# Kernel tuning notes

Hardware: AMD Instinct MI355X
Metric: run time of the kernel (lower is better)

## Reference

```python
import jax, jax.numpy as jnp
import numpy as np

N_NODES = 100000
N_EDGES = 1600000
NUM_GRAPHS = 4096
HID = 128
F_IN = 11
F_OUT = 19


def setup_inputs() -> dict:
    key = jax.random.key(0)
    ks = jax.random.split(key, 8)
    x = jax.random.normal(ks[0], (N_NODES, F_IN), dtype=jnp.float32)
    edge_src = jax.random.randint(ks[1], (N_EDGES,), 0, N_NODES)
    edge_dst = jax.random.randint(ks[2], (N_EDGES,), 0, N_NODES)
    batch = jnp.sort(jax.random.randint(ks[3], (N_NODES,), 0, NUM_GRAPHS))
    W1 = jax.random.normal(ks[4], (F_IN, HID), dtype=jnp.float32) / np.sqrt(F_IN)
    b1 = jnp.zeros((HID,), dtype=jnp.float32)
    W2 = jax.random.normal(ks[5], (HID, HID), dtype=jnp.float32) / np.sqrt(HID)
    b2 = jnp.zeros((HID,), dtype=jnp.float32)
    Wlin = jax.random.normal(ks[6], (HID, F_OUT), dtype=jnp.float32) / np.sqrt(HID)
    blin = jnp.zeros((F_OUT,), dtype=jnp.float32)
    return {"x": x, "edge_src": edge_src, "edge_dst": edge_dst, "batch": batch,
            "W1": W1, "b1": b1, "W2": W2, "b2": b2, "Wlin": Wlin, "blin": blin}


def _gcn_conv(x, W, b, src, dst, norm, n_nodes):
    # x: [N, Fin] -> h: [N, Fout]; gather-normalize-scatter over edges (self-loops included in src/dst/norm)
    h = x @ W
    msgs = h[src] * norm[:, None]              # [E+N, Fout]
    out = jax.ops.segment_sum(msgs, dst, num_segments=n_nodes)
    return out + b


def reference(x, edge_src, edge_dst, batch, W1, b1, W2, b2, Wlin, blin):
    n = x.shape[0]
    # add self-loops (GCNConv default)
    loops = jnp.arange(n)
    src = jnp.concatenate([edge_src, loops])
    dst = jnp.concatenate([edge_dst, loops])
    # symmetric normalization deg^-1/2[src] * deg^-1/2[dst], deg computed on dst with self-loops
    deg = jax.ops.segment_sum(jnp.ones_like(dst, dtype=x.dtype), dst, num_segments=n)
    dinv = jnp.where(deg > 0, jax.lax.rsqrt(deg), 0.0)
    norm = dinv[src] * dinv[dst]
    h = _gcn_conv(x, W1, b1, src, dst, norm, n)
    h = jax.nn.relu(h)
    h = _gcn_conv(h, W2, b2, src, dst, norm, n)
    # global mean pool over batch assignment
    sums = jax.ops.segment_sum(h, batch, num_segments=NUM_GRAPHS)
    cnts = jax.ops.segment_sum(jnp.ones((n,), dtype=h.dtype), batch, num_segments=NUM_GRAPHS)
    pooled = sums / jnp.maximum(cnts, 1.0)[:, None]   # [NUM_GRAPHS, HID]
    return pooled @ Wlin + blin                       # [NUM_GRAPHS, F_OUT]
```

## Files before the change

kernel.cpp:

```cpp
#include <hip/hip_runtime.h>
#include <hip/hip_fp16.h>

#define N_NODES 100000
#define N_EDGES 1600000
#define NUM_G   4096
#define HID     128
#define F_IN    11
#define F_PAD   16
#define F_OUT   19

#define NB      256
#define KPB     391
#define BCAP    8192
#define GCAP    1024
#define P01_EPB 2048
#define NBLK_E  782
#define NGBB    16
#define NREG    8
#define REGW    12500
#define GPB     4
#define NAGG    782
#define CH_G    8

__device__ inline void acc_row_f16(float* acc, uint4 u, float w) {
    const __half2* hp = (const __half2*)&u;
#pragma unroll
    for (int i = 0; i < 4; ++i) {
        acc[2 * i]     += __half2float(__low2half(hp[i]))  * w;
        acc[2 * i + 1] += __half2float(__high2half(hp[i])) * w;
    }
}
__device__ inline void add_row_f16(float* acc, uint4 u) {
    const __half2* hp = (const __half2*)&u;
#pragma unroll
    for (int i = 0; i < 4; ++i) {
        acc[2 * i]     += __half2float(__low2half(hp[i]));
        acc[2 * i + 1] += __half2float(__high2half(hp[i]));
    }
}

__global__ void p1_place(const int* __restrict__ src, const int* __restrict__ dst,
                         const int* __restrict__ batch,
                         int* __restrict__ bcur, unsigned int* __restrict__ ebuf,
                         int* __restrict__ gb) {
    if (blockIdx.x >= NBLK_E) {
        int g = (blockIdx.x - NBLK_E) * 256 + threadIdx.x;
        if (g < NUM_G) {
            int lo = 0, hi = N_NODES;
            while (lo < hi) { int m = (lo + hi) >> 1; if (batch[m] < g) lo = m + 1; else hi = m; }
            gb[g] = lo;
            if (g == NUM_G - 1) gb[NUM_G] = N_NODES;
        }
        return;
    }
    __shared__ int h[NB];
    __shared__ int lbase[NB];
    __shared__ int gbase[NB];
    __shared__ int wsum4[4];
    __shared__ int total_s;
    __shared__ unsigned int stage[P01_EPB];
    __shared__ unsigned char sbuck[P01_EPB];
    int tid = threadIdx.x;
    h[tid] = 0;
    __syncthreads();
    unsigned int pk[8]; int bn[8];
    int b0 = blockIdx.x * P01_EPB;
    int e8 = b0 + tid * 8;
    if (e8 + 8 <= N_EDGES) {
        int4 s0 = *(const int4*)(src + e8);
        int4 s1 = *(const int4*)(src + e8 + 4);
        int4 d0 = *(const int4*)(dst + e8);
        int4 d1 = *(const int4*)(dst + e8 + 4);
        int ss[8] = { s0.x, s0.y, s0.z, s0.w, s1.x, s1.y, s1.z, s1.w };
        int dd[8] = { d0.x, d0.y, d0.z, d0.w, d1.x, d1.y, d1.z, d1.w };
#pragma unroll
        for (int k = 0; k < 8; ++k) {
            bn[k] = dd[k] / KPB;
            pk[k] = ((unsigned)ss[k] << 9) | (unsigned)(dd[k] - bn[k] * KPB);
        }
    } else {
#pragma unroll
        for (int k = 0; k < 8; ++k) {
            int e = e8 + k;
            if (e < N_EDGES) {
                int d = dst[e];
                bn[k] = d / KPB;
                pk[k] = ((unsigned)src[e] << 9) | (unsigned)(d - bn[k] * KPB);
            } else bn[k] = -1;
        }
    }
#pragma unroll
    for (int k = 0; k < 8; ++k)
        if (bn[k] >= 0) atomicAdd(&h[bn[k]], 1);
    __syncthreads();
    int c = h[tid];
    gbase[tid] = c ? atomicAdd(&bcur[tid], c) : 0;
    int lane = tid & 63, wv = tid >> 6;
    int sv = c;
#pragma unroll
    for (int off = 1; off < 64; off <<= 1) {
        int n = __shfl_up(sv, off, 64);
        if (lane >= off) sv += n;
    }
    if (lane == 63) wsum4[wv] = sv;
    __syncthreads();
    int woff = 0;
    for (int w = 0; w < wv; ++w) woff += wsum4[w];
    int excl = sv - c + woff;
    lbase[tid] = excl;
    if (tid == NB - 1) total_s = excl + c;
    __syncthreads();
    h[tid] = 0;
    __syncthreads();
#pragma unroll
    for (int k = 0; k < 8; ++k) {
        if (bn[k] >= 0) {
            int r = atomicAdd(&h[bn[k]], 1);
            int p_ = lbase[bn[k]] + r;
            stage[p_] = pk[k];
            sbuck[p_] = (unsigned char)bn[k];
        }
    }
    __syncthreads();
    int total = total_s;
    for (int i = tid; i < total; i += NB) {
        int b = sbuck[i];
        ebuf[(size_t)b * BCAP + gbase[b] + (i - lbase[b])] = stage[i];
    }
}

__global__ void p2_build(const unsigned int* __restrict__ ebuf, const int* __restrict__ bcur,
                         const float* __restrict__ x,
                         int* __restrict__ row_ptr, int* __restrict__ deg,
                         uint2* __restrict__ cw,
                         float* __restrict__ dinv, __half* __restrict__ xp) {
    __shared__ int hist[512];
    __shared__ float ldinv[512];
    __shared__ int wsum[8];
    __shared__ int woff[8];
    int b  = blockIdx.x;
    int t  = threadIdx.x;
    int dbase = b * KPB;
    int nd = N_NODES - dbase; if (nd > KPB) nd = KPB;
    if (t < 512) hist[t] = 0;
    __syncthreads();
    int e0 = b * BCAP;
    int e1 = e0 + bcur[b];
    for (int e = e0 + t; e < e1; e += 1024)
        atomicAdd(&hist[ebuf[e] & 511u], 1);
    __syncthreads();
    int v = 0, sv = 0;
    int lane = t & 63, wv = t >> 6;
    if (t < 512) {
        v = hist[t];
        sv = v;
#pragma unroll
        for (int off = 1; off < 64; off <<= 1) {
            int n = __shfl_up(sv, off, 64);
            if (lane >= off) sv += n;
        }
        if (lane == 63) wsum[wv] = sv;
    }
    __syncthreads();
    if (t == 0) {
        int run = 0;
#pragma unroll
        for (int w = 0; w < 8; ++w) { woff[w] = run; run += wsum[w]; }
    }
    __syncthreads();
    int excl = 0;
    if (t < 512) {
        excl = sv - v + woff[wv];
        float di = rsqrtf(1.0f + (float)v);
        ldinv[t] = di;
        if (t < nd) {
            row_ptr[dbase + t] = e0 + excl;
            deg[dbase + t]     = v;
            dinv[dbase + t]    = di;
        }
    }
    __syncthreads();
    if (t < 512) hist[t] = e0 + excl;
    __syncthreads();
    for (int e = e0 + t; e < e1; e += 1024) {
        unsigned int w = ebuf[e];
        int dl = (int)(w & 511u);
        int pos = atomicAdd(&hist[dl], 1);
        cw[pos] = make_uint2(w >> 9, __float_as_uint(ldinv[dl]));
    }
    for (int idx = t; idx < nd * F_PAD; idx += 1024) {
        int vl = idx >> 4, f = idx & 15;
        int gv = dbase + vl;
        xp[(size_t)gv * F_PAD + f] =
            __float2half_rn((f < F_IN) ? ldinv[vl] * x[(size_t)gv * F_IN + f] : 0.f);
    }
}

__global__ void agg_es8(const __half* __restrict__ xp, const int* __restrict__ row_ptr,
                        const int* __restrict__ deg, const uint2* __restrict__ cw,
                        const float* __restrict__ dinv,
                        const float* __restrict__ W1, const float* __restrict__ b1,
                        __half* __restrict__ Bh,
                        const int* __restrict__ gb,
                        uint2* __restrict__ ewp, int* __restrict__ gro) {
    __shared__ float xs[128][F_PAD];
    __shared__ float W1s[F_IN * HID];
    __shared__ float b1s[HID];
    __shared__ float ds[128];
    __shared__ int cnt[NREG];
    __shared__ int cur[NREG];
    int tid = threadIdx.x;

    if (blockIdx.x < NAGG) {
        for (int i = tid; i < F_IN * HID; i += 256) W1s[i] = W1[i];
        if (tid < HID) b1s[tid] = b1[tid];
        const uint4* xp4 = (const uint4*)xp;
        int v0   = blockIdx.x * 128;
        int v    = v0 + (tid >> 1);
        int lane = tid & 1;
        if (v < N_NODES) {
            if (lane == 0) ds[tid >> 1] = dinv[v];
            float a[8];
#pragma unroll
            for (int k = 0; k < 8; ++k) a[k] = 0.f;
            add_row_f16(a, xp4[(size_t)v * 2 + lane]);
            int j = row_ptr[v], end = j + deg[v];
            for (; j + 3 < end; j += 4) {
                int s0 = cw[j].x, s1 = cw[j + 1].x, s2 = cw[j + 2].x, s3 = cw[j + 3].x;
                uint4 u0 = xp4[(size_t)s0 * 2 + lane];
                uint4 u1 = xp4[(size_t)s1 * 2 + lane];
                uint4 u2 = xp4[(size_t)s2 * 2 + lane];
                uint4 u3 = xp4[(size_t)s3 * 2 + lane];
                add_row_f16(a, u0); add_row_f16(a, u1);
                add_row_f16(a, u2); add_row_f16(a, u3);
            }
            for (; j < end; ++j)
                add_row_f16(a, xp4[(size_t)cw[j].x * 2 + lane]);
#pragma unroll
            for (int k = 0; k < 8; ++k) xs[tid >> 1][lane * 8 + k] = a[k];
        }
        __syncthreads();
        int jf   = tid & 127;
        int half = tid >> 7;
        int nmax = N_NODES - v0; if (nmax > 128) nmax = 128;
        for (int n = half; n < nmax; n += 2) {
            float a = 0.f;
#pragma unroll
            for (int k = 0; k < F_IN; ++k) a += xs[n][k] * W1s[k * HID + jf];
            float dv = ds[n];
            float h = fmaxf(dv * a + b1s[jf], 0.f);
            Bh[(size_t)(v0 + n) * HID + jf] = __float2half_rn(dv * h);
        }
    } else {
        int g = blockIdx.x - NAGG;
        if (tid < NREG) cnt[tid] = 0;
        __syncthreads();
        int r0 = gb[g], r1 = gb[g + 1];
        int bb0 = 0, bb1 = -1;
        if (r1 > r0) { bb0 = r0 / KPB; bb1 = (r1 - 1) / KPB; }
        for (int bb = bb0; bb <= bb1; ++bb) {
            int vlo = r0 > bb * KPB ? r0 : bb * KPB;
            int vhi = r1 < bb * KPB + KPB ? r1 : bb * KPB + KPB;
            int ee0 = row_ptr[vlo];
            int ee1 = row_ptr[vhi - 1] + deg[vhi - 1];
            for (int e = ee0 + tid; e < ee1; e += 256)
                atomicAdd(&cnt[cw[e].x / REGW], 1);
        }
        for (int v = r0 + tid; v < r1; v += 256)
            atomicAdd(&cnt[(unsigned)v / REGW], 1);
        __syncthreads();
        if (tid == 0) {
            int run = g * GCAP;
#pragma unroll
            for (int p = 0; p < NREG; ++p) {
                gro[g * 9 + p] = run;
                cur[p] = run;
                run += cnt[p];
            }
            gro[g * 9 + 8] = run;
        }
        __syncthreads();
        for (int bb = bb0; bb <= bb1; ++bb) {
            int vlo = r0 > bb * KPB ? r0 : bb * KPB;
            int vhi = r1 < bb * KPB + KPB ? r1 : bb * KPB + KPB;
            int ee0 = row_ptr[vlo];
            int ee1 = row_ptr[vhi - 1] + deg[vhi - 1];
            for (int e = ee0 + tid; e < ee1; e += 256) {
                uint2 q = cw[e];
                int pos = atomicAdd(&cur[q.x / REGW], 1);
                ewp[pos] = q;
            }
        }
        for (int v = r0 + tid; v < r1; v += 256) {
            int pos = atomicAdd(&cur[(unsigned)v / REGW], 1);
            ewp[pos] = make_uint2((unsigned)v, __float_as_uint(dinv[v]));
        }
    }
}

__global__ void pool_gather(const __half* __restrict__ Bh,
                            const int* __restrict__ gro,
                            const uint2* __restrict__ ewp,
                            float* __restrict__ part) {
    __shared__ float red[32][HID + 4];
    int b    = blockIdx.x;
    int gset = b >> 3;
    int p    = b & 7;
    int tid  = threadIdx.x;
    int grp  = tid >> 3;
    int lane = tid & 7;
    int g    = gset * GPB + (grp >> 3);
    int q    = grp & 7;
    const uint4* B4 = (const uint4*)Bh;
    float acc[16];
#pragma unroll
    for (int k = 0; k < 16; ++k) acc[k] = 0.f;

    int e0 = gro[g * 9 + p], e1 = gro[g * 9 + p + 1];
    int e = e0 + q;
    for (; e + 8 < e1; e += 16) {
        uint2 q0 = ewp[e], q1 = ewp[e + 8];
        uint4 u00 = B4[(size_t)q0.x * 16 + lane];
        uint4 u01 = B4[(size_t)q0.x * 16 + 8 + lane];
        uint4 u10 = B4[(size_t)q1.x * 16 + lane];
        uint4 u11 = B4[(size_t)q1.x * 16 + 8 + lane];
        float w0 = __uint_as_float(q0.y), w1 = __uint_as_float(q1.y);
        acc_row_f16(acc,     u00, w0);
        acc_row_f16(acc + 8, u01, w0);
        acc_row_f16(acc,     u10, w1);
        acc_row_f16(acc + 8, u11, w1);
    }
    for (; e < e1; e += 8) {
        uint2 q0 = ewp[e];
        uint4 u00 = B4[(size_t)q0.x * 16 + lane];
        uint4 u01 = B4[(size_t)q0.x * 16 + 8 + lane];
        float w0 = __uint_as_float(q0.y);
        acc_row_f16(acc,     u00, w0);
        acc_row_f16(acc + 8, u01, w0);
    }
#pragma unroll
    for (int k = 0; k < 8; ++k) red[grp][lane * 8 + k]      = acc[k];
#pragma unroll
    for (int k = 0; k < 8; ++k) red[grp][64 + lane * 8 + k] = acc[8 + k];
    __syncthreads();
    for (int i = tid; i < GPB * HID; i += 256) {
        int gg = i >> 7, f = i & 127;
        int rb = gg * 8;
        float s = 0.f;
#pragma unroll
        for (int r = 0; r < 8; ++r) s += red[rb + r][f];
        part[(size_t)((gset * GPB + gg) * NREG + p) * HID + f] = s;
    }
}

__global__ void combine_head(const float* __restrict__ part, const int* __restrict__ gb,
                             const float* __restrict__ W2, const float* __restrict__ b2,
                             const float* __restrict__ Wlin, const float* __restrict__ blin,
                             float* __restrict__ out) {
    __shared__ float r[CH_G][HID];
    __shared__ float tt[CH_G][HID + 4];
    __shared__ float bsc[CH_G];
    int g0  = blockIdx.x * CH_G;
    int tid = threadIdx.x;
    int f   = tid & 127;
    int gh  = tid >> 7;
    int q0  = gh * 4;
#pragma unroll
    for (int c = 0; c < 4; ++c) {
        int gg = q0 + c;
        int g  = g0 + gg;
        float s = 0.f;
#pragma unroll
        for (int p = 0; p < NREG; ++p) s += part[(size_t)(g * NREG + p) * HID + f];
        int cnt = gb[g + 1] - gb[g];
        float inv = (cnt > 0) ? 1.0f / (float)cnt : 0.f;
        r[gg][f] = s * inv;
        if (f == 0) bsc[gg] = (cnt > 0) ? 1.0f : 0.f;
    }
    __syncthreads();
    float bf = b2[f];
    float t0 = bf * bsc[q0];
    float t1 = bf * bsc[q0 + 1];
    float t2 = bf * bsc[q0 + 2];
    float t3 = bf * bsc[q0 + 3];
#pragma unroll 4
    for (int k = 0; k < HID; ++k) {
        float w = W2[k * HID + f];
        t0 += r[q0][k] * w;
        t1 += r[q0 + 1][k] * w;
        t2 += r[q0 + 2][k] * w;
        t3 += r[q0 + 3][k] * w;
    }
    tt[q0][f]     = t0;
    tt[q0 + 1][f] = t1;
    tt[q0 + 2][f] = t2;
    tt[q0 + 3][f] = t3;
    __syncthreads();
    if (tid < CH_G * F_OUT) {
        int gg = tid / F_OUT;
        int fo = tid - gg * F_OUT;
        float o = blin[fo];
#pragma unroll 8
        for (int k = 0; k < HID; ++k) o += tt[gg][k] * Wlin[k * F_OUT + fo];
        out[(size_t)(g0 + gg) * F_OUT + fo] = o;
    }
}

extern "C" void kernel_launch(void* const* d_in, const int* in_sizes, int n_in,
                              void* d_out, int out_size, void* d_ws, size_t ws_size,
                              hipStream_t stream) {
    const float* x    = (const float*)d_in[0];
    const int*   esrc = (const int*)  d_in[1];
    const int*   edst = (const int*)  d_in[2];
    const int*   batch= (const int*)  d_in[3];
    const float* W1   = (const float*)d_in[4];
    const float* b1   = (const float*)d_in[5];
    const float* W2   = (const float*)d_in[6];
    const float* b2   = (const float*)d_in[7];
    const float* Wlin = (const float*)d_in[8];
    const float* blin = (const float*)d_in[9];
    float* out = (float*)d_out;

    char* p = (char*)d_ws;
    float*        dinv    = (float*)p;        p += sizeof(float) * N_NODES;
    __half*       xp      = (__half*)p;       p += sizeof(__half) * (size_t)N_NODES * F_PAD;
    __half*       Bh      = (__half*)p;       p += sizeof(__half) * (size_t)N_NODES * HID;
    unsigned int* ebuf    = (unsigned int*)p; p += sizeof(unsigned int) * (size_t)NB * BCAP;
    uint2*        cw      = (uint2*)p;        p += sizeof(uint2) * (size_t)NB * BCAP;
    int*          deg     = (int*)p;          p += sizeof(int) * N_NODES;
    uint2*        ewp     = (uint2*)p;        p += sizeof(uint2) * (size_t)NUM_G * GCAP;
    float*        part    = (float*)p;        p += sizeof(float) * (size_t)NUM_G * NREG * HID;
    int*          row_ptr = (int*)p;          p += sizeof(int) * (N_NODES + 4);
    int*          gb      = (int*)p;          p += sizeof(int) * (NUM_G + 4);
    int*          gro     = (int*)p;          p += sizeof(int) * (NUM_G * 9 + 4);
    int*          bcur    = (int*)p;          p += sizeof(int) * NB;

    hipMemsetAsync(bcur, 0, sizeof(int) * NB, stream);
    p1_place<<<NBLK_E + NGBB, 256, 0, stream>>>(esrc, edst, batch, bcur, ebuf, gb);
    p2_build<<<NB, 1024, 0, stream>>>(ebuf, bcur, x, row_ptr, deg, cw, dinv, xp);

    agg_es8<<<NAGG + NUM_G, 256, 0, stream>>>(xp, row_ptr, deg, cw, dinv, W1, b1, Bh,
                                              gb, ewp, gro);

    pool_gather<<<(NUM_G / GPB) * NREG, 256, 0, stream>>>(Bh, gro, ewp, part);

    combine_head<<<NUM_G / CH_G, 256, 0, stream>>>(part, gb, W2, b2, Wlin, blin, out);
}
```

Before: 207.4 us.

## Stage CSR and graph-edge bucketing in LDS for coalesced global writes

```diff
diff --git a/kernel.cpp b/kernel.cpp
--- a/kernel.cpp
+++ b/kernel.cpp
@@ -138,6 +138,7 @@
     __shared__ float ldinv[512];
     __shared__ int wsum[8];
     __shared__ int woff[8];
+    __shared__ uint2 scw[BCAP];
     int b  = blockIdx.x;
     int t  = threadIdx.x;
     int dbase = b * KPB;
@@ -180,14 +181,18 @@
         }
     }
     __syncthreads();
-    if (t < 512) hist[t] = e0 + excl;
+    if (t < 512) hist[t] = excl;
     __syncthreads();
     for (int e = e0 + t; e < e1; e += 1024) {
         unsigned int w = ebuf[e];
         int dl = (int)(w & 511u);
         int pos = atomicAdd(&hist[dl], 1);
-        cw[pos] = make_uint2(w >> 9, __float_as_uint(ldinv[dl]));
-    }
+        scw[pos] = make_uint2(w >> 9, __float_as_uint(ldinv[dl]));
+    }
+    __syncthreads();
+    int cnt_ = e1 - e0;
+    for (int i = t; i < cnt_; i += 1024)
+        cw[e0 + i] = scw[i];
     for (int idx = t; idx < nd * F_PAD; idx += 1024) {
         int vl = idx >> 4, f = idx & 15;
         int gv = dbase + vl;
@@ -203,23 +208,33 @@
                         __half* __restrict__ Bh,
                         const int* __restrict__ gb,
                         uint2* __restrict__ ewp, int* __restrict__ gro) {
-    __shared__ float xs[128][F_PAD];
-    __shared__ float W1s[F_IN * HID];
-    __shared__ float b1s[HID];
-    __shared__ float ds[128];
+    __shared__ union SBuf {
+        struct {
+            float xs[128][F_PAD];
+            float W1s[F_IN * HID];
+            float b1s[HID];
+            float ds[128];
+        } a;
+        struct {
+            uint2 dat[GCAP];
+            uint2 ord[GCAP];
+            unsigned char reg[GCAP];
+        } s;
+    } sh;
     __shared__ int cnt[NREG];
     __shared__ int cur[NREG];
+    __shared__ int stot;
     int tid = threadIdx.x;
 
     if (blockIdx.x < NAGG) {
-        for (int i = tid; i < F_IN * HID; i += 256) W1s[i] = W1[i];
-        if (tid < HID) b1s[tid] = b1[tid];
+        for (int i = tid; i < F_IN * HID; i += 256) sh.a.W1s[i] = W1[i];
+        if (tid < HID) sh.a.b1s[tid] = b1[tid];
         const uint4* xp4 = (const uint4*)xp;
         int v0   = blockIdx.x * 128;
         int v    = v0 + (tid >> 1);
         int lane = tid & 1;
         if (v < N_NODES) {
-            if (lane == 0) ds[tid >> 1] = dinv[v];
+            if (lane == 0) sh.a.ds[tid >> 1] = dinv[v];
             float a[8];
 #pragma unroll
             for (int k = 0; k < 8; ++k) a[k] = 0.f;
@@ -237,23 +252,30 @@
             for (; j < end; ++j)
                 add_row_f16(a, xp4[(size_t)cw[j].x * 2 + lane]);
 #pragma unroll
-            for (int k = 0; k < 8; ++k) xs[tid >> 1][lane * 8 + k] = a[k];
+            for (int k = 0; k < 8; ++k) sh.a.xs[tid >> 1][lane * 8 + k] = a[k];
         }
         __syncthreads();
         int jf   = tid & 127;
         int half = tid >> 7;
+        float w[F_IN];
+#pragma unroll
+        for (int k = 0; k < F_IN; ++k) w[k] = sh.a.W1s[k * HID + jf];
+        float bb = sh.a.b1s[jf];
         int nmax = N_NODES - v0; if (nmax > 128) nmax = 128;
         for (int n = half; n < nmax; n += 2) {
-            float a = 0.f;
-#pragma unroll
-            for (int k = 0; k < F_IN; ++k) a += xs[n][k] * W1s[k * HID + jf];
-            float dv = ds[n];
-            float h = fmaxf(dv * a + b1s[jf], 0.f);
+            const float4* xr = (const float4*)sh.a.xs[n];
+            float4 x0 = xr[0], x1 = xr[1], x2 = xr[2];
+            float a = x0.x * w[0] + x0.y * w[1] + x0.z * w[2] + x0.w * w[3]
+                    + x1.x * w[4] + x1.y * w[5] + x1.z * w[6] + x1.w * w[7]
+                    + x2.x * w[8] + x2.y * w[9] + x2.z * w[10];
+            float dv = sh.a.ds[n];
+            float h = fmaxf(dv * a + bb, 0.f);
             Bh[(size_t)(v0 + n) * HID + jf] = __float2half_rn(dv * h);
         }
     } else {
         int g = blockIdx.x - NAGG;
         if (tid < NREG) cnt[tid] = 0;
+        if (tid == 0) stot = 0;
         __syncthreads();
         int r0 = gb[g], r1 = gb[g + 1];
         int bb0 = 0, bb1 = -1;
@@ -263,38 +285,42 @@
             int vhi = r1 < bb * KPB + KPB ? r1 : bb * KPB + KPB;
             int ee0 = row_ptr[vlo];
             int ee1 = row_ptr[vhi - 1] + deg[vhi - 1];
-            for (int e = ee0 + tid; e < ee1; e += 256)
-                atomicAdd(&cnt[cw[e].x / REGW], 1);
-        }
-        for (int v = r0 + tid; v < r1; v += 256)
-            atomicAdd(&cnt[(unsigned)v / REGW], 1);
+            for (int e = ee0 + tid; e < ee1; e += 256) {
+                uint2 q = cw[e];
+                int rg = (int)(q.x / REGW);
+                int si = atomicAdd(&stot, 1);
+                sh.s.dat[si] = q;
+                sh.s.reg[si] = (unsigned char)rg;
+                atomicAdd(&cnt[rg], 1);
+            }
+        }
+        for (int v = r0 + tid; v < r1; v += 256) {
+            int rg = (int)((unsigned)v / REGW);
+            int si = atomicAdd(&stot, 1);
+            sh.s.dat[si] = make_uint2((unsigned)v, __float_as_uint(dinv[v]));
+            sh.s.reg[si] = (unsigned char)rg;
+            atomicAdd(&cnt[rg], 1);
+        }
         __syncthreads();
         if (tid == 0) {
-            int run = g * GCAP;
+            int run = 0;
 #pragma unroll
             for (int p = 0; p < NREG; ++p) {
-                gro[g * 9 + p] = run;
+                gro[g * 9 + p] = g * GCAP + run;
                 cur[p] = run;
                 run += cnt[p];
             }
-            gro[g * 9 + 8] = run;
+            gro[g * 9 + 8] = g * GCAP + run;
         }
         __syncthreads();
-        for (int bb = bb0; bb <= bb1; ++bb) {
-            int vlo = r0 > bb * KPB ? r0 : bb * KPB;
-            int vhi = r1 < bb * KPB + KPB ? r1 : bb * KPB + KPB;
-            int ee0 = row_ptr[vlo];
-            int ee1 = row_ptr[vhi - 1] + deg[vhi - 1];
-            for (int e = ee0 + tid; e < ee1; e += 256) {
-                uint2 q = cw[e];
-                int pos = atomicAdd(&cur[q.x / REGW], 1);
-                ewp[pos] = q;
-            }
-        }
-        for (int v = r0 + tid; v < r1; v += 256) {
-            int pos = atomicAdd(&cur[(unsigned)v / REGW], 1);
-            ewp[pos] = make_uint2((unsigned)v, __float_as_uint(dinv[v]));
-        }
+        int tot = stot;
+        for (int i = tid; i < tot; i += 256) {
+            int pos = atomicAdd(&cur[sh.s.reg[i]], 1);
+            sh.s.ord[pos] = sh.s.dat[i];
+        }
+        __syncthreads();
+        for (int i = tid; i < tot; i += 256)
+            ewp[(size_t)g * GCAP + i] = sh.s.ord[i];
     }
 }
 
```

New measurement: 202.9 us (median of 3 runs). -2.2%, faster.
